# Kernel tuning notes

Hardware: AMD Instinct MI355X
Metric: run time of the kernel (lower is better)

The kernel has to match this reference:

```python
import jax, jax.numpy as jnp
import numpy as np

D, A, V, H, FFH = 512, 256, 256, 1, 256
B, S, VOCAB = 4096, 50, 100000


def _layer_norm(x, g, b, eps=1e-6):
    mu = jnp.mean(x, axis=-1, keepdims=True)
    var = jnp.mean((x - mu) ** 2, axis=-1, keepdims=True)
    return (x - mu) / jnp.sqrt(var + eps) * g + b


def setup_inputs() -> dict:
    key = jax.random.key(0)
    ks = jax.random.split(key, 12)
    s = 0.02
    return {
        "embed_table": jax.random.normal(ks[0], (VOCAB, D), jnp.float32),
        "idx": jax.random.randint(ks[1], (B, S), 0, VOCAB, dtype=jnp.int32),
        "lengths": jax.random.randint(ks[2], (B,), 0, S, dtype=jnp.int32),
        "W1": jax.random.normal(ks[3], (D, FFH), jnp.float32) * s,
        "b1": jnp.zeros((FFH,), jnp.float32),
        "W2": jax.random.normal(ks[4], (FFH, D), jnp.float32) * s,
        "b2": jnp.zeros((D,), jnp.float32),
        "ln1_g": jnp.ones((D,), jnp.float32),
        "ln1_b": jnp.zeros((D,), jnp.float32),
        "W_qkv": jax.random.normal(ks[5], (D, 2 * A + V), jnp.float32) * s,
        "b_qkv": jnp.zeros((2 * A + V,), jnp.float32),
        "W_o": jax.random.normal(ks[6], (V, D), jnp.float32) * s,
        "b_o": jnp.zeros((D,), jnp.float32),
        "ln2_g": jnp.ones((D,), jnp.float32),
        "ln2_b": jnp.zeros((D,), jnp.float32),
    }


def reference(embed_table, idx, lengths, W1, b1, W2, b2, ln1_g, ln1_b,
              W_qkv, b_qkv, W_o, b_o, ln2_g, ln2_b):
    # neighbor validity mask; guaranteed >= 1 valid neighbor per node
    mask = jnp.arange(S)[None, :] <= lengths[:, None]          # [B,S] bool

    # irregular gather of neighbor embeddings into padded tensor
    x = embed_table[idx]                                       # [B,S,D]

    # FeedForward (relu -> linear) + residual + LayerNorm
    ff = jnp.maximum(jnp.einsum('bsd,df->bsf', x, W1) + b1, 0.0)
    ff = jnp.einsum('bsf,fd->bsd', ff, W2) + b2
    ff = _layer_norm(ff + x, ln1_g, ln1_b)                     # [B,S,D]

    # MultiHeadSelfAttention (combined QKV projection)
    qkv = jnp.einsum('bsd,dc->bsc', ff, W_qkv) + b_qkv         # [B,S,2A+V]
    q, k, v = qkv[..., :A], qkv[..., A:2 * A], qkv[..., 2 * A:]
    q = q.reshape(B, S, H, A // H)
    k = k.reshape(B, S, H, A // H)
    v = v.reshape(B, S, H, V // H)
    scale = jnp.asarray(np.sqrt(D // H), q.dtype)              # AllenNLP scale
    scores = jnp.einsum('bqhd,bkhd->bhqk', q / scale, k)       # [B,H,S,S]
    scores = jnp.where(mask[:, None, None, :], scores, jnp.asarray(-1e9, scores.dtype))
    attn = jax.nn.softmax(scores, axis=-1)
    ctx = jnp.einsum('bhqk,bkhd->bqhd', attn, v).reshape(B, S, V)
    attn_out = jnp.einsum('bsv,vd->bsd', ctx, W_o) + b_o

    out = _layer_norm(attn_out + ff, ln2_g, ln2_b)             # [B,S,D]

    # masked mean pool over neighbors
    m = mask[..., None].astype(out.dtype)                      # [B,S,1]
    pooled = jnp.sum(out * m, axis=1) / jnp.maximum(jnp.sum(m, axis=1), 1e-13)
    return pooled                                              # [B,D]
```

## Files before the change

### kernel.cpp

```cpp
#include <hip/hip_runtime.h>

typedef __bf16 bf16x8 __attribute__((ext_vector_type(8)));
typedef float float4v __attribute__((ext_vector_type(4)));
typedef unsigned short ushort4v __attribute__((ext_vector_type(4)));
typedef unsigned short ushort8v __attribute__((ext_vector_type(8)));

#define K_D 512
#define K_S 50

__device__ __forceinline__ float b2f(unsigned short u) {
  union { unsigned int u32; float f; } v; v.u32 = ((unsigned int)u) << 16; return v.f;
}
__device__ __forceinline__ unsigned short f2b(float f) {
  __bf16 h = (__bf16)f;
  return __builtin_bit_cast(unsigned short, h);
}

__device__ __forceinline__ bf16x8 ldfrag(const unsigned short* buf, int E, int r0, int k0, int lane) {
  int row = r0 + (lane & 15);
  int kb = (k0 + ((lane >> 4) << 3)) << 1;
  return *(const bf16x8*)(buf + row * E + ((kb ^ ((row & 7) << 4)) >> 1));
}
__device__ __forceinline__ bf16x8 ldfragm(const unsigned short* buf, int E, int r0, int k0,
                                          int lane, int mask) {
  int row = r0 + (lane & 15);
  int kb = (k0 + ((lane >> 4) << 3)) << 1;
  return *(const bf16x8*)(buf + row * E + ((kb ^ ((row & mask) << 4)) >> 1));
}

__device__ __forceinline__ float4v mfma16(bf16x8 a, bf16x8 b, float4v c) {
  return __builtin_amdgcn_mfma_f32_16x16x32_bf16(a, b, c, 0, 0, 0);
}

__global__ void prep_weights(const float* __restrict__ src, unsigned short* __restrict__ dst,
                             int K, int N) {
  int KT = K >> 5;
  int total = (N >> 4) * KT * 64;
  int t = blockIdx.x * blockDim.x + threadIdx.x;
  if (t >= total) return;
  int l = t & 63;
  int kt = (t >> 6) % KT;
  int nt = (t >> 6) / KT;
  int kbase = kt * 32 + ((l >> 4) << 3);
  int col = nt * 16 + (l & 15);
  ushort8v o;
  #pragma unroll
  for (int j = 0; j < 8; ++j) o[j] = f2b(src[(size_t)(kbase + j) * N + col]);
  *(ushort8v*)(dst + (size_t)t * 8) = o;
}

__global__ void zero_meta(int* meta) { if (threadIdx.x < 2) meta[threadIdx.x] = 0; }

__global__ void bucket(const int* __restrict__ lengths, int* __restrict__ lists,
                       int* __restrict__ meta) {
  int i = blockIdx.x * blockDim.x + threadIdx.x;
  if (i >= 4096) return;
  int mt = (lengths[i] + 16) >> 4;
  if (mt <= 2) { int p = atomicAdd(&meta[0], 1); lists[p] = i; }
  else         { int p = atomicAdd(&meta[1], 1); lists[4096 + p] = i; }
}

template<int NT, int KS, int MT, int SLOTS, int APRE>
__device__ __forceinline__ void mmN(const unsigned short* Ab, int EA,
                                    const bf16x8* __restrict__ Wf, int wnb, int KT, int l,
                                    float4v* acc) {
  if constexpr (SLOTS == 2) {
    bf16x8 p0[NT], p1[NT];
    #pragma unroll
    for (int n = 0; n < NT; ++n) {
      p0[n] = Wf[(size_t)((wnb + n) * KT) * 64 + l];
      p1[n] = Wf[(size_t)((wnb + n) * KT + 1) * 64 + l];
    }
    bf16x8 a0[MT], a1[MT];
    if constexpr (APRE) {
      #pragma unroll
      for (int m = 0; m < MT; ++m) {
        a0[m] = ldfrag(Ab, EA, m * 16, 0, l);
        a1[m] = ldfrag(Ab, EA, m * 16, 32, l);
      }
    }
    #pragma unroll 1
    for (int kt = 0; kt < KS; kt += 2) {
      {
        if constexpr (!APRE) {
          #pragma unroll
          for (int m = 0; m < MT; ++m) a0[m] = ldfrag(Ab, EA, m * 16, kt * 32, l);
        }
        #pragma unroll
        for (int n = 0; n < NT; ++n) {
          #pragma unroll
          for (int m = 0; m < MT; ++m)
            acc[m * NT + n] = mfma16(a0[m], p0[n], acc[m * NT + n]);
        }
        if (kt + 2 < KS) {
          #pragma unroll
          for (int n = 0; n < NT; ++n)
            p0[n] = Wf[(size_t)((wnb + n) * KT + kt + 2) * 64 + l];
          if constexpr (APRE) {
            #pragma unroll
            for (int m = 0; m < MT; ++m) a0[m] = ldfrag(Ab, EA, m * 16, (kt + 2) * 32, l);
          }
        }
      }
      {
        if constexpr (!APRE) {
          #pragma unroll
          for (int m = 0; m < MT; ++m) a1[m] = ldfrag(Ab, EA, m * 16, (kt + 1) * 32, l);
        }
        #pragma unroll
        for (int n = 0; n < NT; ++n) {
          #pragma unroll
          for (int m = 0; m < MT; ++m)
            acc[m * NT + n] = mfma16(a1[m], p1[n], acc[m * NT + n]);
        }
        if (kt + 3 < KS) {
          #pragma unroll
          for (int n = 0; n < NT; ++n)
            p1[n] = Wf[(size_t)((wnb + n) * KT + kt + 3) * 64 + l];
          if constexpr (APRE) {
            #pragma unroll
            for (int m = 0; m < MT; ++m) a1[m] = ldfrag(Ab, EA, m * 16, (kt + 3) * 32, l);
          }
        }
      }
    }
  } else {
    bf16x8 bn[NT];
    #pragma unroll
    for (int n = 0; n < NT; ++n) bn[n] = Wf[(size_t)((wnb + n) * KT) * 64 + l];
    #pragma unroll 1
    for (int kt = 0; kt < KS; ++kt) {
      bf16x8 a[MT];
      #pragma unroll
      for (int m = 0; m < MT; ++m) a[m] = ldfrag(Ab, EA, m * 16, kt * 32, l);
      #pragma unroll
      for (int n = 0; n < NT; ++n) {
        #pragma unroll
        for (int m = 0; m < MT; ++m)
          acc[m * NT + n] = mfma16(a[m], bn[n], acc[m * NT + n]);
      }
      if (kt + 1 < KS) {
        #pragma unroll
        for (int n = 0; n < NT; ++n)
          bn[n] = Wf[(size_t)((wnb + n) * KT + kt + 1) * 64 + l];
      }
    }
  }
}

template<int STRIDE>
__device__ __forceinline__ void ln_pass(unsigned short* sXbuf, const float* __restrict__ g,
                                        const float* __restrict__ bb, int widx, int l, int nrows) {
  float gv[8], bv[8];
  {
    const float4* g4 = (const float4*)(g + l * 8);
    const float4* b4 = (const float4*)(bb + l * 8);
    float4 a0 = g4[0], a1 = g4[1], c0 = b4[0], c1 = b4[1];
    gv[0] = a0.x; gv[1] = a0.y; gv[2] = a0.z; gv[3] = a0.w;
    gv[4] = a1.x; gv[5] = a1.y; gv[6] = a1.z; gv[7] = a1.w;
    bv[0] = c0.x; bv[1] = c0.y; bv[2] = c0.z; bv[3] = c0.w;
    bv[4] = c1.x; bv[5] = c1.y; bv[6] = c1.z; bv[7] = c1.w;
  }
  #pragma unroll 1
  for (int r = widx; r < nrows; r += STRIDE) {
    int e = r * 512 + (((l << 4) ^ ((r & 7) << 4)) >> 1);
    ushort8v x = *(const ushort8v*)(sXbuf + e);
    float v[8];
    float s = 0.f, s2 = 0.f;
    #pragma unroll
    for (int j = 0; j < 8; ++j) { v[j] = b2f(x[j]); s += v[j]; s2 += v[j] * v[j]; }
    #pragma unroll
    for (int off = 1; off < 64; off <<= 1) { s += __shfl_xor(s, off); s2 += __shfl_xor(s2, off); }
    float mu = s * (1.f / 512.f);
    float var = s2 * (1.f / 512.f) - mu * mu;
    float rstd = rsqrtf(var + 1e-6f);
    ushort8v o;
    #pragma unroll
    for (int j = 0; j < 8; ++j) o[j] = f2b((v[j] - mu) * rstd * gv[j] + bv[j]);
    *(ushort8v*)(sXbuf + e) = o;
  }
}

__device__ __forceinline__ void qkv_pass(const unsigned short* sX,
                                         const unsigned short* wqkvf, int nt, int l,
                                         unsigned short* sQ, unsigned short* sK,
                                         const float* __restrict__ bqkv, float4v accV[2]) {
  const bf16x8* Wf = (const bf16x8*)wqkvf;
  float4v accQ[2], accK[2];
  accQ[0] = (float4v){0.f,0.f,0.f,0.f}; accQ[1] = accQ[0];
  accK[0] = accQ[0]; accK[1] = accQ[0];
  accV[0] = accQ[0]; accV[1] = accQ[0];
  const size_t bQ = (size_t)(nt) * 16 * 64 + l;
  const size_t bK = (size_t)(16 + nt) * 16 * 64 + l;
  const size_t bV = (size_t)(32 + nt) * 16 * 64 + l;
  bf16x8 q0 = Wf[bQ], k0 = Wf[bK], v0 = Wf[bV];
  #pragma unroll 1
  for (int kt = 0; kt < 16; ++kt) {
    bf16x8 a0 = ldfrag(sX, 512, 0, kt * 32, l);
    bf16x8 a1 = ldfrag(sX, 512, 16, kt * 32, l);
    accQ[0] = mfma16(a0, q0, accQ[0]); accQ[1] = mfma16(a1, q0, accQ[1]);
    accK[0] = mfma16(a0, k0, accK[0]); accK[1] = mfma16(a1, k0, accK[1]);
    accV[0] = mfma16(a0, v0, accV[0]); accV[1] = mfma16(a1, v0, accV[1]);
    if (kt + 1 < 16) {
      q0 = Wf[bQ + (size_t)(kt + 1) * 64];
      k0 = Wf[bK + (size_t)(kt + 1) * 64];
      v0 = Wf[bV + (size_t)(kt + 1) * 64];
    }
  }
  const float qscale = 0.044194173824159216f;
  int col = nt * 16 + (l & 15);
  float biasQ = bqkv[col];
  float biasK = bqkv[256 + col];
  #pragma unroll
  for (int m = 0; m < 2; ++m) {
    int r0 = m * 16 + ((l >> 4) << 2);
    #pragma unroll
    for (int j = 0; j < 4; ++j) {
      int r = r0 + j;
      sQ[r * 256 + (((col << 1) ^ ((r & 7) << 4)) >> 1)] = f2b((accQ[m][j] + biasQ) * qscale);
      sK[r * 256 + (((col << 1) ^ ((r & 7) << 4)) >> 1)] = f2b(accK[m][j] + biasK);
    }
  }
}

__device__ __forceinline__ void small_body(
    unsigned short* sX, unsigned short* sQ, unsigned short* sK,
    float* sS, unsigned short* sP,
    const float* __restrict__ embed, const int* __restrict__ gidx,
    const float* __restrict__ b1, const float* __restrict__ b2,
    const float* __restrict__ ln1g, const float* __restrict__ ln1b,
    const float* __restrict__ bqkv, const float* __restrict__ bo,
    const float* __restrict__ ln2g, const float* __restrict__ ln2b,
    const unsigned short* __restrict__ w1f, const unsigned short* __restrict__ w2f,
    const unsigned short* __restrict__ wqkvf, const unsigned short* __restrict__ wof,
    float* __restrict__ out, int ht, int ws, int l, int item, int len) {

  {
    int sub = ht >> 7;
    int c0 = (ht & 127) << 2;
    #pragma unroll 2
    for (int it = 0; it < 8; ++it) {
      int r = it * 4 + sub;
      float4 v = make_float4(0.f, 0.f, 0.f, 0.f);
      if (r <= len) {
        int row = gidx[item * K_S + r];
        v = *(const float4*)(embed + (size_t)row * K_D + c0);
      }
      ushort4v o;
      o[0] = f2b(v.x); o[1] = f2b(v.y); o[2] = f2b(v.z); o[3] = f2b(v.w);
      *(ushort4v*)(sX + r * 512 + (((c0 << 1) ^ ((r & 7) << 4)) >> 1)) = o;
    }
  }
  __syncthreads();

  {
    float4v acc[4];
    #pragma unroll
    for (int i = 0; i < 4; ++i) acc[i] = (float4v){0.f,0.f,0.f,0.f};
    mmN<2, 16, 2, 2, 1>(sX, 512, (const bf16x8*)w1f, ws * 2, 16, l, acc);
    #pragma unroll
    for (int n = 0; n < 2; ++n) {
      int col = (ws * 2 + n) * 16 + (l & 15);
      float bias = b1[col];
      #pragma unroll
      for (int m = 0; m < 2; ++m) {
        int r0 = m * 16 + ((l >> 4) << 2);
        #pragma unroll
        for (int j = 0; j < 4; ++j) {
          int r = r0 + j;
          sQ[r * 256 + (((col << 1) ^ ((r & 7) << 4)) >> 1)] = f2b(fmaxf(acc[m * 2 + n][j] + bias, 0.f));
        }
      }
    }
  }
  __syncthreads();

  #pragma unroll 1
  for (int p = 0; p < 2; ++p) {
    float4v acc[4];
    #pragma unroll
    for (int i = 0; i < 4; ++i) acc[i] = (float4v){0.f,0.f,0.f,0.f};
    mmN<2, 8, 2, 2, 1>(sQ, 256, (const bf16x8*)w2f, ws * 4 + p * 2, 8, l, acc);
    #pragma unroll
    for (int n = 0; n < 2; ++n) {
      int col = (ws * 4 + p * 2 + n) * 16 + (l & 15);
      float bias = b2[col];
      #pragma unroll
      for (int m = 0; m < 2; ++m) {
        int r0 = m * 16 + ((l >> 4) << 2);
        #pragma unroll
        for (int j = 0; j < 4; ++j) {
          int r = r0 + j;
          int e = r * 512 + (((col << 1) ^ ((r & 7) << 4)) >> 1);
          sX[e] = f2b(acc[m * 2 + n][j] + bias + b2f(sX[e]));
        }
      }
    }
  }
  __syncthreads();
  ln_pass<8>(sX, ln1g, ln1b, ws, l, 32);
  __syncthreads();

  float4v accV0[2], accV1[2];
  qkv_pass(sX, wqkvf, ws * 2 + 0, l, sQ, sK, bqkv, accV0);
  qkv_pass(sX, wqkvf, ws * 2 + 1, l, sQ, sK, bqkv, accV1);
  __syncthreads();

  if (ws < 4) {
    int m0 = (ws >> 1) * 16, n0 = (ws & 1) * 16;
    float4v acc = (float4v){0.f,0.f,0.f,0.f};
    bf16x8 b0 = ldfrag(sK, 256, n0, 0, l),  aq0 = ldfrag(sQ, 256, m0, 0, l);
    bf16x8 b1 = ldfrag(sK, 256, n0, 32, l), aq1 = ldfrag(sQ, 256, m0, 32, l);
    #pragma unroll 1
    for (int kt = 0; kt < 8; kt += 2) {
      acc = mfma16(aq0, b0, acc);
      if (kt + 2 < 8) { b0 = ldfrag(sK, 256, n0, (kt + 2) * 32, l); aq0 = ldfrag(sQ, 256, m0, (kt + 2) * 32, l); }
      acc = mfma16(aq1, b1, acc);
      if (kt + 3 < 8) { b1 = ldfrag(sK, 256, n0, (kt + 3) * 32, l); aq1 = ldfrag(sQ, 256, m0, (kt + 3) * 32, l); }
    }
    int col = n0 + (l & 15);
    int r0 = m0 + ((l >> 4) << 2);
    #pragma unroll
    for (int j = 0; j < 4; ++j) {
      int r = r0 + j;
      sS[r * 64 + (((col << 2) ^ ((r & 7) << 4)) >> 2)] = acc[j];
    }
  }
  __syncthreads();

  {
    const bool valid = (l <= len);
    #pragma unroll 1
    for (int r = ws; r < 32; r += 8) {
      float s = valid ? sS[r * 64 + (((l << 2) ^ ((r & 7) << 4)) >> 2)] : -1e30f;
      float mx = s;
      #pragma unroll
      for (int off = 1; off < 64; off <<= 1) mx = fmaxf(mx, __shfl_xor(mx, off));
      float p = valid ? __expf(s - mx) : 0.f;
      float sum = p;
      #pragma unroll
      for (int off = 1; off < 64; off <<= 1) sum += __shfl_xor(sum, off);
      sP[r * 64 + (((l << 1) ^ ((r & 7) << 4)) >> 1)] = f2b(p / sum);
    }
    #pragma unroll
    for (int p = 0; p < 2; ++p) {
      int c = (ws * 2 + p) * 16 + (l & 15);
      float biasV = bqkv[512 + c];
      const float4v* aV = p ? accV1 : accV0;
      #pragma unroll
      for (int m = 0; m < 2; ++m) {
        int r0 = m * 16 + ((l >> 4) << 2);
        ushort4v o;
        #pragma unroll
        for (int j = 0; j < 4; ++j) o[j] = f2b(aV[m][j] + biasV);
        *(ushort4v*)(sK + c * 32 + (((r0 << 1) ^ ((c & 3) << 4)) >> 1)) = o;
      }
    }
  }
  __syncthreads();

  {
    bf16x8 pa0 = ldfrag(sP, 64, 0, 0, l);
    bf16x8 pa1 = ldfrag(sP, 64, 16, 0, l);
    bf16x8 bf0 = ldfragm(sK, 32, (ws * 2 + 0) * 16, 0, l, 3);
    bf16x8 bf1 = ldfragm(sK, 32, (ws * 2 + 1) * 16, 0, l, 3);
    float4v z = (float4v){0.f,0.f,0.f,0.f};
    float4v c00 = mfma16(pa0, bf0, z), c10 = mfma16(pa1, bf0, z);
    float4v c01 = mfma16(pa0, bf1, z), c11 = mfma16(pa1, bf1, z);
    #pragma unroll
    for (int p = 0; p < 2; ++p) {
      int col = (ws * 2 + p) * 16 + (l & 15);
      #pragma unroll
      for (int m = 0; m < 2; ++m) {
        const float4v& cc = p ? (m ? c11 : c01) : (m ? c10 : c00);
        int r0 = m * 16 + ((l >> 4) << 2);
        #pragma unroll
        for (int j = 0; j < 4; ++j) {
          int r = r0 + j;
          sQ[r * 256 + (((col << 1) ^ ((r & 7) << 4)) >> 1)] = f2b(cc[j]);
        }
      }
    }
  }
  __syncthreads();

  #pragma unroll 1
  for (int p = 0; p < 2; ++p) {
    float4v acc[4];
    #pragma unroll
    for (int i = 0; i < 4; ++i) acc[i] = (float4v){0.f,0.f,0.f,0.f};
    mmN<2, 8, 2, 2, 1>(sQ, 256, (const bf16x8*)wof, ws * 4 + p * 2, 8, l, acc);
    #pragma unroll
    for (int n = 0; n < 2; ++n) {
      int col = (ws * 4 + p * 2 + n) * 16 + (l & 15);
      float bias = bo[col];
      #pragma unroll
      for (int m = 0; m < 2; ++m) {
        int r0 = m * 16 + ((l >> 4) << 2);
        #pragma unroll
        for (int j = 0; j < 4; ++j) {
          int r = r0 + j;
          int e = r * 512 + (((col << 1) ^ ((r & 7) << 4)) >> 1);
          sX[e] = f2b(acc[m * 2 + n][j] + bias + b2f(sX[e]));
        }
      }
    }
  }
  __syncthreads();
  ln_pass<8>(sX, ln2g, ln2b, ws, l, 32);
  __syncthreads();

  {
    float sum = 0.f;
    for (int s = 0; s <= len; ++s)
      sum += b2f(sX[s * 512 + (((ht << 1) ^ ((s & 7) << 4)) >> 1)]);
    out[(size_t)item * K_D + ht] = sum / (float)(len + 1);
  }
}

template<int MT>
__device__ __forceinline__ void big_body(
    unsigned short* sX, unsigned short* sQ, unsigned short* sK,
    float* sS, unsigned short* sP,
    const float* __restrict__ embed, const int* __restrict__ gidx,
    const float* __restrict__ b1, const float* __restrict__ b2,
    const float* __restrict__ ln1g, const float* __restrict__ ln1b,
    const float* __restrict__ bqkv, const float* __restrict__ bo,
    const float* __restrict__ ln2g, const float* __restrict__ ln2b,
    const unsigned short* __restrict__ w1f, const unsigned short* __restrict__ w2f,
    const unsigned short* __restrict__ wqkvf, const unsigned short* __restrict__ wof,
    float* __restrict__ out, int tid, int w, int l, int item, int len) {

  constexpr int ROWS = 16 * MT;
  constexpr int S2 = (MT <= 3) ? 2 : 1;
  constexpr int AP1 = (MT <= 3) ? 1 : 0;

  {
    const int sub = tid >> 7;
    const int c0 = (tid & 127) << 2;
    #pragma unroll 2
    for (int it = 0; it < 2 * MT; ++it) {
      int r = it * 8 + sub;
      float4 v = make_float4(0.f, 0.f, 0.f, 0.f);
      if (r <= len) {
        int row = gidx[item * K_S + r];
        v = *(const float4*)(embed + (size_t)row * K_D + c0);
      }
      ushort4v o;
      o[0] = f2b(v.x); o[1] = f2b(v.y); o[2] = f2b(v.z); o[3] = f2b(v.w);
      *(ushort4v*)(sX + r * 512 + (((c0 << 1) ^ ((r & 7) << 4)) >> 1)) = o;
    }
  }
  __syncthreads();

  {
    float4v acc[MT];
    #pragma unroll
    for (int i = 0; i < MT; ++i) acc[i] = (float4v){0.f,0.f,0.f,0.f};
    mmN<1, 16, MT, 2, AP1>(sX, 512, (const bf16x8*)w1f, w, 16, l, acc);
    int col = w * 16 + (l & 15);
    float bias = b1[col];
    #pragma unroll
    for (int m = 0; m < MT; ++m) {
      int r0 = m * 16 + ((l >> 4) << 2);
      #pragma unroll
      for (int j = 0; j < 4; ++j) {
        int r = r0 + j;
        sQ[r * 256 + (((col << 1) ^ ((r & 7) << 4)) >> 1)] = f2b(fmaxf(acc[m][j] + bias, 0.f));
      }
    }
  }
  __syncthreads();

  {
    float4v acc[2 * MT];
    #pragma unroll
    for (int i = 0; i < 2 * MT; ++i) acc[i] = (float4v){0.f,0.f,0.f,0.f};
    mmN<2, 8, MT, S2, 0>(sQ, 256, (const bf16x8*)w2f, w * 2, 8, l, acc);
    #pragma unroll
    for (int n = 0; n < 2; ++n) {
      int col = (w * 2 + n) * 16 + (l & 15);
      float bias = b2[col];
      #pragma unroll
      for (int m = 0; m < MT; ++m) {
        int r0 = m * 16 + ((l >> 4) << 2);
        #pragma unroll
        for (int j = 0; j < 4; ++j) {
          int r = r0 + j;
          int e = r * 512 + (((col << 1) ^ ((r & 7) << 4)) >> 1);
          sX[e] = f2b(acc[m * 2 + n][j] + bias + b2f(sX[e]));
        }
      }
    }
  }
  __syncthreads();
  ln_pass<16>(sX, ln1g, ln1b, w, l, ROWS);
  __syncthreads();

  {
    const bf16x8* Wf = (const bf16x8*)wqkvf;
    float4v accQ[MT], accK[MT];
    #pragma unroll
    for (int i = 0; i < MT; ++i) {
      accQ[i] = (float4v){0.f,0.f,0.f,0.f};
      accK[i] = (float4v){0.f,0.f,0.f,0.f};
    }
    const size_t baseQ = (size_t)(w) * 16 * 64 + l;
    const size_t baseK = (size_t)(16 + w) * 16 * 64 + l;
    bf16x8 q0 = Wf[baseQ], k0 = Wf[baseK];
    #pragma unroll 1
    for (int kt = 0; kt < 16; ++kt) {
      bf16x8 a[MT];
      #pragma unroll
      for (int m = 0; m < MT; ++m) a[m] = ldfrag(sX, 512, m * 16, kt * 32, l);
      #pragma unroll
      for (int m = 0; m < MT; ++m) accQ[m] = mfma16(a[m], q0, accQ[m]);
      #pragma unroll
      for (int m = 0; m < MT; ++m) accK[m] = mfma16(a[m], k0, accK[m]);
      if (kt + 1 < 16) {
        q0 = Wf[baseQ + (size_t)(kt + 1) * 64];
        k0 = Wf[baseK + (size_t)(kt + 1) * 64];
      }
    }
    const float qscale = 0.044194173824159216f;
    int col = w * 16 + (l & 15);
    float biasQ = bqkv[col];
    float biasK = bqkv[256 + col];
    #pragma unroll
    for (int m = 0; m < MT; ++m) {
      int r0 = m * 16 + ((l >> 4) << 2);
      #pragma unroll
      for (int j = 0; j < 4; ++j) {
        int r = r0 + j;
        sQ[r * 256 + (((col << 1) ^ ((r & 7) << 4)) >> 1)] = f2b((accQ[m][j] + biasQ) * qscale);
        sK[r * 256 + (((col << 1) ^ ((r & 7) << 4)) >> 1)] = f2b(accK[m][j] + biasK);
      }
    }
  }
  __syncthreads();

  if ((w >> 2) < MT) {
    float4v acc = (float4v){0.f,0.f,0.f,0.f};
    int n0 = (w & 3) * 16;
    int m0 = (w >> 2) * 16;
    bf16x8 b0 = ldfrag(sK, 256, n0, 0, l),  aq0 = ldfrag(sQ, 256, m0, 0, l);
    bf16x8 b1 = ldfrag(sK, 256, n0, 32, l), aq1 = ldfrag(sQ, 256, m0, 32, l);
    #pragma unroll 1
    for (int kt = 0; kt < 8; kt += 2) {
      acc = mfma16(aq0, b0, acc);
      if (kt + 2 < 8) { b0 = ldfrag(sK, 256, n0, (kt + 2) * 32, l); aq0 = ldfrag(sQ, 256, m0, (kt + 2) * 32, l); }
      acc = mfma16(aq1, b1, acc);
      if (kt + 3 < 8) { b1 = ldfrag(sK, 256, n0, (kt + 3) * 32, l); aq1 = ldfrag(sQ, 256, m0, (kt + 3) * 32, l); }
    }
    int col = n0 + (l & 15);
    int r0 = m0 + ((l >> 4) << 2);
    #pragma unroll
    for (int j = 0; j < 4; ++j) {
      int r = r0 + j;
      sS[r * 64 + (((col << 2) ^ ((r & 7) << 4)) >> 2)] = acc[j];
    }
  }
  float4v accV[MT];
  {
    #pragma unroll
    for (int i = 0; i < MT; ++i) accV[i] = (float4v){0.f,0.f,0.f,0.f};
    mmN<1, 16, MT, 2, AP1>(sX, 512, (const bf16x8*)wqkvf, 32 + w, 16, l, accV);
  }
  __syncthreads();

  {
    const bool valid = (l <= len);
    #pragma unroll 1
    for (int r = w; r < ROWS; r += 16) {
      float s = valid ? sS[r * 64 + (((l << 2) ^ ((r & 7) << 4)) >> 2)] : -1e30f;
      float mx = s;
      #pragma unroll
      for (int off = 1; off < 64; off <<= 1) mx = fmaxf(mx, __shfl_xor(mx, off));
      float p = valid ? __expf(s - mx) : 0.f;
      float sum = p;
      #pragma unroll
      for (int off = 1; off < 64; off <<= 1) sum += __shfl_xor(sum, off);
      sP[r * 64 + (((l << 1) ^ ((r & 7) << 4)) >> 1)] = f2b(p / sum);
    }
    int c = w * 16 + (l & 15);
    float biasV = bqkv[512 + c];
    #pragma unroll
    for (int m = 0; m < MT; ++m) {
      int r0 = m * 16 + ((l >> 4) << 2);
      ushort4v o;
      #pragma unroll
      for (int j = 0; j < 4; ++j) o[j] = f2b(accV[m][j] + biasV);
      *(ushort4v*)(sK + c * 64 + (((r0 << 1) ^ ((c & 7) << 4)) >> 1)) = o;
    }
    #pragma unroll
    for (int m = MT; m < 4; ++m) {
      int r0 = m * 16 + ((l >> 4) << 2);
      ushort4v o; o[0] = 0; o[1] = 0; o[2] = 0; o[3] = 0;
      *(ushort4v*)(sK + c * 64 + (((r0 << 1) ^ ((c & 7) << 4)) >> 1)) = o;
    }
  }
  __syncthreads();

  {
    float4v acc[MT];
    #pragma unroll
    for (int i = 0; i < MT; ++i) acc[i] = (float4v){0.f,0.f,0.f,0.f};
    #pragma unroll
    for (int kt = 0; kt < 2; ++kt) {
      bf16x8 bfr = ldfragm(sK, 64, w * 16, kt * 32, l, 7);
      #pragma unroll
      for (int m = 0; m < MT; ++m) {
        bf16x8 a = ldfrag(sP, 64, m * 16, kt * 32, l);
        acc[m] = mfma16(a, bfr, acc[m]);
      }
    }
    int col = w * 16 + (l & 15);
    #pragma unroll
    for (int m = 0; m < MT; ++m) {
      int r0 = m * 16 + ((l >> 4) << 2);
      #pragma unroll
      for (int j = 0; j < 4; ++j) {
        int r = r0 + j;
        sQ[r * 256 + (((col << 1) ^ ((r & 7) << 4)) >> 1)] = f2b(acc[m][j]);
      }
    }
  }
  __syncthreads();

  {
    float4v acc[2 * MT];
    #pragma unroll
    for (int i = 0; i < 2 * MT; ++i) acc[i] = (float4v){0.f,0.f,0.f,0.f};
    mmN<2, 8, MT, S2, 0>(sQ, 256, (const bf16x8*)wof, w * 2, 8, l, acc);
    #pragma unroll
    for (int n = 0; n < 2; ++n) {
      int col = (w * 2 + n) * 16 + (l & 15);
      float bias = bo[col];
      #pragma unroll
      for (int m = 0; m < MT; ++m) {
        int r0 = m * 16 + ((l >> 4) << 2);
        #pragma unroll
        for (int j = 0; j < 4; ++j) {
          int r = r0 + j;
          int e = r * 512 + (((col << 1) ^ ((r & 7) << 4)) >> 1);
          sX[e] = f2b(acc[m * 2 + n][j] + bias + b2f(sX[e]));
        }
      }
    }
  }
  __syncthreads();
  ln_pass<16>(sX, ln2g, ln2b, w, l, ROWS);
  __syncthreads();

  {
    int col = tid & 511;
    int half = tid >> 9;
    float sum = 0.f;
    for (int s = half; s <= len; s += 2)
      sum += b2f(sX[s * 512 + (((col << 1) ^ ((s & 7) << 4)) >> 1)]);
    if (half) sS[col] = sum;
    __syncthreads();
    if (!half) out[(size_t)item * K_D + col] = (sum + sS[col]) / (float)(len + 1);
  }
}

__global__ __launch_bounds__(1024, 4)
void fused_all(
    const float* __restrict__ embed, const int* __restrict__ gidx,
    const int* __restrict__ lengths,
    const float* __restrict__ b1, const float* __restrict__ b2,
    const float* __restrict__ ln1g, const float* __restrict__ ln1b,
    const float* __restrict__ bqkv, const float* __restrict__ bo,
    const float* __restrict__ ln2g, const float* __restrict__ ln2b,
    const unsigned short* __restrict__ w1f, const unsigned short* __restrict__ w2f,
    const unsigned short* __restrict__ wqkvf, const unsigned short* __restrict__ wof,
    const int* __restrict__ lists, const int* __restrict__ meta,
    float* __restrict__ out) {
  __shared__ unsigned char lds[155648];

  const int tid = (int)threadIdx.x;
  const int w = tid >> 6;
  const int l = tid & 63;
  const int j = (int)blockIdx.x;
  const int nsmall = meta[0];
  const int nbig = meta[1];

  if (j < 2048) {
    if (2 * j >= nsmall) return;
    int i0 = lists[2 * j];
    int i1 = (2 * j + 1 < nsmall) ? lists[2 * j + 1] : i0;
    int h = w >> 3;
    int ws = w & 7;
    int ht = ws * 64 + l;
    int item = h ? i1 : i0;
    int len = lengths[item];
    size_t base = (size_t)h * 77824;
    unsigned short* sX = (unsigned short*)(lds + base);
    unsigned short* sQ = (unsigned short*)(lds + base + 32768);
    unsigned short* sK = (unsigned short*)(lds + base + 49152);
    float* sS = (float*)(lds + base + 65536);
    unsigned short* sP = (unsigned short*)(lds + base + 73728);
    small_body(sX, sQ, sK, sS, sP, embed, gidx, b1, b2, ln1g, ln1b, bqkv, bo,
               ln2g, ln2b, w1f, w2f, wqkvf, wof, out, ht, ws, l, item, len);
  } else {
    int bi = j - 2048;
    if (bi >= nbig) return;
    int item = lists[4096 + bi];
    int len = lengths[item];
    int mt = (len + 16) >> 4;
    unsigned short* sX = (unsigned short*)lds;
    unsigned short* sQ = (unsigned short*)(lds + 65536);
    unsigned short* sK = (unsigned short*)(lds + 98304);
    float* sS = (float*)(lds + 131072);
    unsigned short* sP = (unsigned short*)(lds + 147456);
    if (mt == 3)
      big_body<3>(sX, sQ, sK, sS, sP, embed, gidx, b1, b2, ln1g, ln1b, bqkv, bo,
                  ln2g, ln2b, w1f, w2f, wqkvf, wof, out, tid, w, l, item, len);
    else
      big_body<4>(sX, sQ, sK, sS, sP, embed, gidx, b1, b2, ln1g, ln1b, bqkv, bo,
                  ln2g, ln2b, w1f, w2f, wqkvf, wof, out, tid, w, l, item, len);
  }
}

extern "C" void kernel_launch(void* const* d_in, const int* in_sizes, int n_in,
                              void* d_out, int out_size, void* d_ws, size_t ws_size,
                              hipStream_t stream) {
  (void)in_sizes; (void)n_in; (void)out_size; (void)ws_size;
  const float* embed = (const float*)d_in[0];
  const int* idx = (const int*)d_in[1];
  const int* lengths = (const int*)d_in[2];
  const float* W1 = (const float*)d_in[3];
  const float* b1 = (const float*)d_in[4];
  const float* W2 = (const float*)d_in[5];
  const float* b2 = (const float*)d_in[6];
  const float* ln1g = (const float*)d_in[7];
  const float* ln1b = (const float*)d_in[8];
  const float* Wqkv = (const float*)d_in[9];
  const float* bqkv = (const float*)d_in[10];
  const float* Wo = (const float*)d_in[11];
  const float* bo = (const float*)d_in[12];
  const float* ln2g = (const float*)d_in[13];
  const float* ln2b = (const float*)d_in[14];

  unsigned short* ws = (unsigned short*)d_ws;
  unsigned short* w1f = ws;
  unsigned short* w2f = ws + 131072;
  unsigned short* wqkvf = ws + 262144;
  unsigned short* wof = ws + 655360;
  int* lists = (int*)(ws + 786432);
  int* meta = lists + 8192;

  prep_weights<<<64, 256, 0, stream>>>(W1, w1f, 512, 256);
  prep_weights<<<64, 256, 0, stream>>>(W2, w2f, 256, 512);
  prep_weights<<<192, 256, 0, stream>>>(Wqkv, wqkvf, 512, 768);
  prep_weights<<<64, 256, 0, stream>>>(Wo, wof, 256, 512);
  zero_meta<<<1, 64, 0, stream>>>(meta);
  bucket<<<16, 256, 0, stream>>>(lengths, lists, meta);

  fused_all<<<6144, 1024, 0, stream>>>(embed, idx, lengths, b1, b2, ln1g, ln1b,
                                       bqkv, bo, ln2g, ln2b, w1f, w2f, wqkvf, wof,
                                       lists, meta, (float*)d_out);
}
```

Baseline: 499.6 us.

## Add a single-tile bucket for short items and specialize the small body on tile count

Lengths are now split into three buckets (one tile, two tiles, more). The small-item path is templated on the number of 16-row tiles, so items with at most 16 rows run every GEMM, LayerNorm and attention step on one tile instead of two. The FF1 stage is also restructured to compute one column tile per pass, and the block grid is shrunk to the new maximum of paired plus big blocks. This is meant to cut wasted MFMA and LDS work on padded rows, at the cost of more template code and an extra zero-fill of unused V rows.

```diff
diff --git a/kernel.cpp b/kernel.cpp
--- a/kernel.cpp
+++ b/kernel.cpp
@@ -49,15 +49,16 @@
   *(ushort8v*)(dst + (size_t)t * 8) = o;
 }
 
-__global__ void zero_meta(int* meta) { if (threadIdx.x < 2) meta[threadIdx.x] = 0; }
+__global__ void zero_meta(int* meta) { if (threadIdx.x < 3) meta[threadIdx.x] = 0; }
 
 __global__ void bucket(const int* __restrict__ lengths, int* __restrict__ lists,
                        int* __restrict__ meta) {
   int i = blockIdx.x * blockDim.x + threadIdx.x;
   if (i >= 4096) return;
   int mt = (lengths[i] + 16) >> 4;
-  if (mt <= 2) { int p = atomicAdd(&meta[0], 1); lists[p] = i; }
-  else         { int p = atomicAdd(&meta[1], 1); lists[4096 + p] = i; }
+  if (mt == 1)      { int p = atomicAdd(&meta[0], 1); lists[p] = i; }
+  else if (mt == 2) { int p = atomicAdd(&meta[1], 1); lists[4096 + p] = i; }
+  else              { int p = atomicAdd(&meta[2], 1); lists[8192 + p] = i; }
 }
 
 template<int NT, int KS, int MT, int SLOTS, int APRE>
@@ -181,26 +182,34 @@
   }
 }
 
+template<int MT>
 __device__ __forceinline__ void qkv_pass(const unsigned short* sX,
                                          const unsigned short* wqkvf, int nt, int l,
                                          unsigned short* sQ, unsigned short* sK,
-                                         const float* __restrict__ bqkv, float4v accV[2]) {
+                                         const float* __restrict__ bqkv, float4v accV[MT]) {
   const bf16x8* Wf = (const bf16x8*)wqkvf;
-  float4v accQ[2], accK[2];
-  accQ[0] = (float4v){0.f,0.f,0.f,0.f}; accQ[1] = accQ[0];
-  accK[0] = accQ[0]; accK[1] = accQ[0];
-  accV[0] = accQ[0]; accV[1] = accQ[0];
+  float4v accQ[MT], accK[MT];
+  #pragma unroll
+  for (int m = 0; m < MT; ++m) {
+    accQ[m] = (float4v){0.f,0.f,0.f,0.f};
+    accK[m] = accQ[m];
+    accV[m] = accQ[m];
+  }
   const size_t bQ = (size_t)(nt) * 16 * 64 + l;
   const size_t bK = (size_t)(16 + nt) * 16 * 64 + l;
   const size_t bV = (size_t)(32 + nt) * 16 * 64 + l;
   bf16x8 q0 = Wf[bQ], k0 = Wf[bK], v0 = Wf[bV];
   #pragma unroll 1
   for (int kt = 0; kt < 16; ++kt) {
-    bf16x8 a0 = ldfrag(sX, 512, 0, kt * 32, l);
-    bf16x8 a1 = ldfrag(sX, 512, 16, kt * 32, l);
-    accQ[0] = mfma16(a0, q0, accQ[0]); accQ[1] = mfma16(a1, q0, accQ[1]);
-    accK[0] = mfma16(a0, k0, accK[0]); accK[1] = mfma16(a1, k0, accK[1]);
-    accV[0] = mfma16(a0, v0, accV[0]); accV[1] = mfma16(a1, v0, accV[1]);
+    bf16x8 a[MT];
+    #pragma unroll
+    for (int m = 0; m < MT; ++m) a[m] = ldfrag(sX, 512, m * 16, kt * 32, l);
+    #pragma unroll
+    for (int m = 0; m < MT; ++m) accQ[m] = mfma16(a[m], q0, accQ[m]);
+    #pragma unroll
+    for (int m = 0; m < MT; ++m) accK[m] = mfma16(a[m], k0, accK[m]);
+    #pragma unroll
+    for (int m = 0; m < MT; ++m) accV[m] = mfma16(a[m], v0, accV[m]);
     if (kt + 1 < 16) {
       q0 = Wf[bQ + (size_t)(kt + 1) * 64];
       k0 = Wf[bK + (size_t)(kt + 1) * 64];
@@ -212,7 +221,7 @@
   float biasQ = bqkv[col];
   float biasK = bqkv[256 + col];
   #pragma unroll
-  for (int m = 0; m < 2; ++m) {
+  for (int m = 0; m < MT; ++m) {
     int r0 = m * 16 + ((l >> 4) << 2);
     #pragma unroll
     for (int j = 0; j < 4; ++j) {
@@ -223,6 +232,7 @@
   }
 }
 
+template<int MT>
 __device__ __forceinline__ void small_body(
     unsigned short* sX, unsigned short* sQ, unsigned short* sK,
     float* sS, unsigned short* sP,
@@ -235,11 +245,13 @@
     const unsigned short* __restrict__ wqkvf, const unsigned short* __restrict__ wof,
     float* __restrict__ out, int ht, int ws, int l, int item, int len) {
 
+  constexpr int ROWS = 16 * MT;
+
   {
     int sub = ht >> 7;
     int c0 = (ht & 127) << 2;
     #pragma unroll 2
-    for (int it = 0; it < 8; ++it) {
+    for (int it = 0; it < 4 * MT; ++it) {
       int r = it * 4 + sub;
       float4 v = make_float4(0.f, 0.f, 0.f, 0.f);
       if (r <= len) {
@@ -253,40 +265,39 @@
   }
   __syncthreads();
 
-  {
-    float4v acc[4];
-    #pragma unroll
-    for (int i = 0; i < 4; ++i) acc[i] = (float4v){0.f,0.f,0.f,0.f};
-    mmN<2, 16, 2, 2, 1>(sX, 512, (const bf16x8*)w1f, ws * 2, 16, l, acc);
-    #pragma unroll
-    for (int n = 0; n < 2; ++n) {
-      int col = (ws * 2 + n) * 16 + (l & 15);
-      float bias = b1[col];
-      #pragma unroll
-      for (int m = 0; m < 2; ++m) {
-        int r0 = m * 16 + ((l >> 4) << 2);
-        #pragma unroll
-        for (int j = 0; j < 4; ++j) {
-          int r = r0 + j;
-          sQ[r * 256 + (((col << 1) ^ ((r & 7) << 4)) >> 1)] = f2b(fmaxf(acc[m * 2 + n][j] + bias, 0.f));
-        }
-      }
-    }
-  }
-  __syncthreads();
-
   #pragma unroll 1
   for (int p = 0; p < 2; ++p) {
-    float4v acc[4];
-    #pragma unroll
-    for (int i = 0; i < 4; ++i) acc[i] = (float4v){0.f,0.f,0.f,0.f};
-    mmN<2, 8, 2, 2, 1>(sQ, 256, (const bf16x8*)w2f, ws * 4 + p * 2, 8, l, acc);
+    int nt = ws * 2 + p;
+    float4v acc[MT];
+    #pragma unroll
+    for (int i = 0; i < MT; ++i) acc[i] = (float4v){0.f,0.f,0.f,0.f};
+    mmN<1, 16, MT, 2, 1>(sX, 512, (const bf16x8*)w1f, nt, 16, l, acc);
+    int col = nt * 16 + (l & 15);
+    float bias = b1[col];
+    #pragma unroll
+    for (int m = 0; m < MT; ++m) {
+      int r0 = m * 16 + ((l >> 4) << 2);
+      #pragma unroll
+      for (int j = 0; j < 4; ++j) {
+        int r = r0 + j;
+        sQ[r * 256 + (((col << 1) ^ ((r & 7) << 4)) >> 1)] = f2b(fmaxf(acc[m][j] + bias, 0.f));
+      }
+    }
+  }
+  __syncthreads();
+
+  #pragma unroll 1
+  for (int p = 0; p < 2; ++p) {
+    float4v acc[2 * MT];
+    #pragma unroll
+    for (int i = 0; i < 2 * MT; ++i) acc[i] = (float4v){0.f,0.f,0.f,0.f};
+    mmN<2, 8, MT, 2, 1>(sQ, 256, (const bf16x8*)w2f, ws * 4 + p * 2, 8, l, acc);
     #pragma unroll
     for (int n = 0; n < 2; ++n) {
       int col = (ws * 4 + p * 2 + n) * 16 + (l & 15);
       float bias = b2[col];
       #pragma unroll
-      for (int m = 0; m < 2; ++m) {
+      for (int m = 0; m < MT; ++m) {
         int r0 = m * 16 + ((l >> 4) << 2);
         #pragma unroll
         for (int j = 0; j < 4; ++j) {
@@ -298,32 +309,37 @@
     }
   }
   __syncthreads();
-  ln_pass<8>(sX, ln1g, ln1b, ws, l, 32);
-  __syncthreads();
-
-  float4v accV0[2], accV1[2];
-  qkv_pass(sX, wqkvf, ws * 2 + 0, l, sQ, sK, bqkv, accV0);
-  qkv_pass(sX, wqkvf, ws * 2 + 1, l, sQ, sK, bqkv, accV1);
-  __syncthreads();
-
-  if (ws < 4) {
-    int m0 = (ws >> 1) * 16, n0 = (ws & 1) * 16;
-    float4v acc = (float4v){0.f,0.f,0.f,0.f};
-    bf16x8 b0 = ldfrag(sK, 256, n0, 0, l),  aq0 = ldfrag(sQ, 256, m0, 0, l);
-    bf16x8 b1 = ldfrag(sK, 256, n0, 32, l), aq1 = ldfrag(sQ, 256, m0, 32, l);
-    #pragma unroll 1
-    for (int kt = 0; kt < 8; kt += 2) {
-      acc = mfma16(aq0, b0, acc);
-      if (kt + 2 < 8) { b0 = ldfrag(sK, 256, n0, (kt + 2) * 32, l); aq0 = ldfrag(sQ, 256, m0, (kt + 2) * 32, l); }
-      acc = mfma16(aq1, b1, acc);
-      if (kt + 3 < 8) { b1 = ldfrag(sK, 256, n0, (kt + 3) * 32, l); aq1 = ldfrag(sQ, 256, m0, (kt + 3) * 32, l); }
-    }
-    int col = n0 + (l & 15);
-    int r0 = m0 + ((l >> 4) << 2);
-    #pragma unroll
-    for (int j = 0; j < 4; ++j) {
-      int r = r0 + j;
-      sS[r * 64 + (((col << 2) ^ ((r & 7) << 4)) >> 2)] = acc[j];
+  ln_pass<8>(sX, ln1g, ln1b, ws, l, ROWS);
+  __syncthreads();
+
+  float4v accV0[MT], accV1[MT];
+  qkv_pass<MT>(sX, wqkvf, ws * 2 + 0, l, sQ, sK, bqkv, accV0);
+  qkv_pass<MT>(sX, wqkvf, ws * 2 + 1, l, sQ, sK, bqkv, accV1);
+  __syncthreads();
+
+  {
+    bool doS;
+    int m0, n0;
+    if constexpr (MT == 1) { doS = (ws == 0); m0 = 0; n0 = 0; }
+    else                   { doS = (ws < 4); m0 = (ws >> 1) * 16; n0 = (ws & 1) * 16; }
+    if (doS) {
+      float4v acc = (float4v){0.f,0.f,0.f,0.f};
+      bf16x8 b0 = ldfrag(sK, 256, n0, 0, l),  aq0 = ldfrag(sQ, 256, m0, 0, l);
+      bf16x8 b1 = ldfrag(sK, 256, n0, 32, l), aq1 = ldfrag(sQ, 256, m0, 32, l);
+      #pragma unroll 1
+      for (int kt = 0; kt < 8; kt += 2) {
+        acc = mfma16(aq0, b0, acc);
+        if (kt + 2 < 8) { b0 = ldfrag(sK, 256, n0, (kt + 2) * 32, l); aq0 = ldfrag(sQ, 256, m0, (kt + 2) * 32, l); }
+        acc = mfma16(aq1, b1, acc);
+        if (kt + 3 < 8) { b1 = ldfrag(sK, 256, n0, (kt + 3) * 32, l); aq1 = ldfrag(sQ, 256, m0, (kt + 3) * 32, l); }
+      }
+      int col = n0 + (l & 15);
+      int r0 = m0 + ((l >> 4) << 2);
+      #pragma unroll
+      for (int j = 0; j < 4; ++j) {
+        int r = r0 + j;
+        sS[r * 64 + (((col << 2) ^ ((r & 7) << 4)) >> 2)] = acc[j];
+      }
     }
   }
   __syncthreads();
@@ -331,7 +347,7 @@
   {
     const bool valid = (l <= len);
     #pragma unroll 1
-    for (int r = ws; r < 32; r += 8) {
+    for (int r = ws; r < ROWS; r += 8) {
       float s = valid ? sS[r * 64 + (((l << 2) ^ ((r & 7) << 4)) >> 2)] : -1e30f;
       float mx = s;
       #pragma unroll
@@ -348,31 +364,37 @@
       float biasV = bqkv[512 + c];
       const float4v* aV = p ? accV1 : accV0;
       #pragma unroll
-      for (int m = 0; m < 2; ++m) {
+      for (int m = 0; m < MT; ++m) {
         int r0 = m * 16 + ((l >> 4) << 2);
         ushort4v o;
         #pragma unroll
         for (int j = 0; j < 4; ++j) o[j] = f2b(aV[m][j] + biasV);
         *(ushort4v*)(sK + c * 32 + (((r0 << 1) ^ ((c & 3) << 4)) >> 1)) = o;
       }
-    }
-  }
-  __syncthreads();
-
-  {
-    bf16x8 pa0 = ldfrag(sP, 64, 0, 0, l);
-    bf16x8 pa1 = ldfrag(sP, 64, 16, 0, l);
+      #pragma unroll
+      for (int m = MT; m < 2; ++m) {
+        int r0 = m * 16 + ((l >> 4) << 2);
+        ushort4v o; o[0] = 0; o[1] = 0; o[2] = 0; o[3] = 0;
+        *(ushort4v*)(sK + c * 32 + (((r0 << 1) ^ ((c & 3) << 4)) >> 1)) = o;
+      }
+    }
+  }
+  __syncthreads();
+
+  {
+    bf16x8 pa[MT];
+    #pragma unroll
+    for (int m = 0; m < MT; ++m) pa[m] = ldfrag(sP, 64, m * 16, 0, l);
     bf16x8 bf0 = ldfragm(sK, 32, (ws * 2 + 0) * 16, 0, l, 3);
     bf16x8 bf1 = ldfragm(sK, 32, (ws * 2 + 1) * 16, 0, l, 3);
     float4v z = (float4v){0.f,0.f,0.f,0.f};
-    float4v c00 = mfma16(pa0, bf0, z), c10 = mfma16(pa1, bf0, z);
-    float4v c01 = mfma16(pa0, bf1, z), c11 = mfma16(pa1, bf1, z);
     #pragma unroll
     for (int p = 0; p < 2; ++p) {
+      const bf16x8& bfr = p ? bf1 : bf0;
       int col = (ws * 2 + p) * 16 + (l & 15);
       #pragma unroll
-      for (int m = 0; m < 2; ++m) {
-        const float4v& cc = p ? (m ? c11 : c01) : (m ? c10 : c00);
+      for (int m = 0; m < MT; ++m) {
+        float4v cc = mfma16(pa[m], bfr, z);
         int r0 = m * 16 + ((l >> 4) << 2);
         #pragma unroll
         for (int j = 0; j < 4; ++j) {
@@ -386,16 +408,16 @@
 
   #pragma unroll 1
   for (int p = 0; p < 2; ++p) {
-    float4v acc[4];
-    #pragma unroll
-    for (int i = 0; i < 4; ++i) acc[i] = (float4v){0.f,0.f,0.f,0.f};
-    mmN<2, 8, 2, 2, 1>(sQ, 256, (const bf16x8*)wof, ws * 4 + p * 2, 8, l, acc);
+    float4v acc[2 * MT];
+    #pragma unroll
+    for (int i = 0; i < 2 * MT; ++i) acc[i] = (float4v){0.f,0.f,0.f,0.f};
+    mmN<2, 8, MT, 2, 1>(sQ, 256, (const bf16x8*)wof, ws * 4 + p * 2, 8, l, acc);
     #pragma unroll
     for (int n = 0; n < 2; ++n) {
       int col = (ws * 4 + p * 2 + n) * 16 + (l & 15);
       float bias = bo[col];
       #pragma unroll
-      for (int m = 0; m < 2; ++m) {
+      for (int m = 0; m < MT; ++m) {
         int r0 = m * 16 + ((l >> 4) << 2);
         #pragma unroll
         for (int j = 0; j < 4; ++j) {
@@ -407,7 +429,7 @@
     }
   }
   __syncthreads();
-  ln_pass<8>(sX, ln2g, ln2b, ws, l, 32);
+  ln_pass<8>(sX, ln2g, ln2b, ws, l, ROWS);
   __syncthreads();
 
   {
@@ -682,30 +704,40 @@
   const int w = tid >> 6;
   const int l = tid & 63;
   const int j = (int)blockIdx.x;
-  const int nsmall = meta[0];
-  const int nbig = meta[1];
-
-  if (j < 2048) {
-    if (2 * j >= nsmall) return;
-    int i0 = lists[2 * j];
-    int i1 = (2 * j + 1 < nsmall) ? lists[2 * j + 1] : i0;
+  const int n1 = meta[0];
+  const int n2 = meta[1];
+  const int nbig = meta[2];
+  const int p1 = (n1 + 1) >> 1;
+  const int p2 = (n2 + 1) >> 1;
+
+  if (j < p1 + p2) {
+    const bool m1 = (j < p1);
+    const int base = m1 ? 0 : 4096;
+    const int cnt = m1 ? n1 : n2;
+    const int jj = m1 ? j : j - p1;
+    int i0 = lists[base + 2 * jj];
+    int i1 = (2 * jj + 1 < cnt) ? lists[base + 2 * jj + 1] : i0;
     int h = w >> 3;
-    int ws = w & 7;
-    int ht = ws * 64 + l;
+    int ws_ = w & 7;
+    int ht = ws_ * 64 + l;
     int item = h ? i1 : i0;
     int len = lengths[item];
-    size_t base = (size_t)h * 77824;
-    unsigned short* sX = (unsigned short*)(lds + base);
-    unsigned short* sQ = (unsigned short*)(lds + base + 32768);
-    unsigned short* sK = (unsigned short*)(lds + base + 49152);
-    float* sS = (float*)(lds + base + 65536);
-    unsigned short* sP = (unsigned short*)(lds + base + 73728);
-    small_body(sX, sQ, sK, sS, sP, embed, gidx, b1, b2, ln1g, ln1b, bqkv, bo,
-               ln2g, ln2b, w1f, w2f, wqkvf, wof, out, ht, ws, l, item, len);
+    size_t bo_ = (size_t)h * 77824;
+    unsigned short* sX = (unsigned short*)(lds + bo_);
+    unsigned short* sQ = (unsigned short*)(lds + bo_ + 32768);
+    unsigned short* sK = (unsigned short*)(lds + bo_ + 49152);
+    float* sS = (float*)(lds + bo_ + 65536);
+    unsigned short* sP = (unsigned short*)(lds + bo_ + 73728);
+    if (m1)
+      small_body<1>(sX, sQ, sK, sS, sP, embed, gidx, b1, b2, ln1g, ln1b, bqkv, bo,
+                    ln2g, ln2b, w1f, w2f, wqkvf, wof, out, ht, ws_, l, item, len);
+    else
+      small_body<2>(sX, sQ, sK, sS, sP, embed, gidx, b1, b2, ln1g, ln1b, bqkv, bo,
+                    ln2g, ln2b, w1f, w2f, wqkvf, wof, out, ht, ws_, l, item, len);
   } else {
-    int bi = j - 2048;
+    int bi = j - (p1 + p2);
     if (bi >= nbig) return;
-    int item = lists[4096 + bi];
+    int item = lists[8192 + bi];
     int len = lengths[item];
     int mt = (len + 16) >> 4;
     unsigned short* sX = (unsigned short*)lds;
@@ -748,7 +780,7 @@
   unsigned short* wqkvf = ws + 262144;
   unsigned short* wof = ws + 655360;
   int* lists = (int*)(ws + 786432);
-  int* meta = lists + 8192;
+  int* meta = lists + 12288;
 
   prep_weights<<<64, 256, 0, stream>>>(W1, w1f, 512, 256);
   prep_weights<<<64, 256, 0, stream>>>(W2, w2f, 256, 512);
@@ -757,7 +789,7 @@
   zero_meta<<<1, 64, 0, stream>>>(meta);
   bucket<<<16, 256, 0, stream>>>(lengths, lists, meta);
 
-  fused_all<<<6144, 1024, 0, stream>>>(embed, idx, lengths, b1, b2, ln1g, ln1b,
+  fused_all<<<4608, 1024, 0, stream>>>(embed, idx, lengths, b1, b2, ln1g, ln1b,
                                        bqkv, bo, ln2g, ln2b, w1f, w2f, wqkvf, wof,
                                        lists, meta, (float*)d_out);
 }
```

Measured after the change: 481.9 us. 3.5% less time.
